# Optimization experiments

Measured on AMD Instinct MI355X. Metric: run time of the kernel, lower is better.

Reference implementation:

```python
import jax, jax.numpy as jnp
import numpy as np

B, S, N, D = 4, 4, 2048, 2048  # batch, residual streams, seq len, model dim


def rmsnorm(x, gamma, eps=1e-12):
    # F.normalize(x, dim=-1) * sqrt(d) * (gamma + 1)
    n = jnp.sqrt(jnp.sum(x * x, axis=-1, keepdims=True))
    return x / jnp.maximum(n, eps) * (x.shape[-1] ** 0.5) * (gamma + 1.0)


def setup_inputs() -> dict:
    key = jax.random.key(0)
    k0, k1, k2, k3 = jax.random.split(key, 4)
    residuals = jax.random.normal(k0, (B * S, N, D), dtype=jnp.float32)
    gamma = (jax.random.normal(k1, (D,), dtype=jnp.float32) * 0.02)
    # ProjActScale weights are zero-init in the module; use small random values
    # so the dynamic paths are numerically exercised.
    w_alpha = jax.random.normal(k2, (S + 1, D), dtype=jnp.float32) * 0.02
    w_beta = jax.random.normal(k3, (1, D), dtype=jnp.float32) * 0.02
    scale_alpha = jnp.asarray(0.01, dtype=jnp.float32)
    scale_beta = jnp.asarray(0.01, dtype=jnp.float32)
    # static_alpha = cat([init_alpha0, eye(S)], dim=1), layer_index=0 -> one-hot row 0
    init_alpha0 = np.zeros((S, 1), dtype=np.float32)
    init_alpha0[0, 0] = 1.0
    static_alpha = jnp.asarray(np.concatenate([init_alpha0, np.eye(S, dtype=np.float32)], axis=1))
    static_beta = jnp.ones((S,), dtype=jnp.float32)
    return dict(residuals=residuals, gamma=gamma, w_alpha=w_alpha, scale_alpha=scale_alpha,
                static_alpha=static_alpha, w_beta=w_beta, scale_beta=scale_beta,
                static_beta=static_beta)


def reference(residuals, gamma, w_alpha, scale_alpha, static_alpha, w_beta, scale_beta, static_beta):
    bs, n, d = residuals.shape
    s = static_beta.shape[0]
    b = bs // s
    # '(b s) n d -> b n s d'
    x = residuals.reshape(b, s, n, d).transpose(0, 2, 1, 3)
    normed = rmsnorm(x, gamma)
    # dynamic alpha / beta: zero-bias linear -> tanh -> scale
    dyn_alpha = jnp.tanh(jnp.einsum('bnsd,td->bnst', normed, w_alpha)) * scale_alpha
    alpha = dyn_alpha + static_alpha                      # (b, n, s, s+1)
    dyn_beta = jnp.tanh(jnp.einsum('bnsd,od->bnso', normed, w_beta))[..., 0] * scale_beta
    beta = dyn_beta + static_beta                         # (b, n, s)
    # width connection: mix residual streams
    mix = jnp.einsum('bnst,bnsd->bntd', alpha, x)         # (b, n, s+1, d)
    branch_input = mix[:, :, 0, :]                        # (b, n, d)
    res = mix[:, :, 1:, :]                                # (b, n, s, d)
    # identity branch (module has branch=None; the add_residual closure applies this)
    branch_out = branch_input
    # depth connection: outer product with beta, add residuals
    res = branch_out[:, :, None, :] * beta[..., None] + res
    # 'b n s d -> (b s) n d'
    out = res.transpose(0, 2, 1, 3).reshape(bs, n, d)
    return out
```

## Files before the change

### kernel.cpp

```cpp
#include <hip/hip_runtime.h>
#include <math.h>

#define NB 4
#define NS 4
#define NN 2048
#define ND 2048
#define NTHREADS 256
#define SQRT_D 45.254833995939045f

typedef float f32x4 __attribute__((ext_vector_type(4)));

#if __has_builtin(__builtin_amdgcn_global_load_lds)
#define HAVE_DMA 1
typedef __attribute__((address_space(3))) void lds_void_t;
typedef const __attribute__((address_space(1))) void glb_void_t;
#define ASYNC_COPY16(g, l) \
    __builtin_amdgcn_global_load_lds((glb_void_t*)(g), (lds_void_t*)(l), 16, 0, 0)
#else
#define HAVE_DMA 0
#endif

#define SHIP(I, H, M_) {                                      \
    const float keep_ = hi_ ? v[(I)+(H)] : v[(I)];            \
    const float give_ = hi_ ? v[(I)] : v[(I)+(H)];            \
    v[(I)] = keep_ + __shfl_xor(give_, (M_)); }

__global__ __launch_bounds__(NTHREADS, 4)
void hyperconn_kernel(const float* __restrict__ residuals,
                      const float* __restrict__ gamma,
                      const float* __restrict__ w_alpha,
                      const float* __restrict__ scale_alpha,
                      const float* __restrict__ static_alpha,
                      const float* __restrict__ w_beta,
                      const float* __restrict__ scale_beta,
                      const float* __restrict__ static_beta,
                      float* __restrict__ out)
{
    __shared__ float lds_x[NS * ND];
    __shared__ float red[4][32];
    __shared__ float asb[NS][6];

    const int tid  = threadIdx.x;
    const int bn   = blockIdx.x;
    const int b    = bn >> 11;
    const int n    = bn & (NN - 1);
    const int wave = tid >> 6;
    const int lane = tid & 63;
    const int d0   = tid << 2;
    const int d1   = d0 + (ND >> 1);

    const size_t row_stride = (size_t)NN * ND;
    const float* xrow = residuals + (size_t)(b * NS + wave) * row_stride + (size_t)n * ND;

#if HAVE_DMA
#pragma unroll
    for (int i = 0; i < 8; ++i) {
        ASYNC_COPY16(xrow + i * 256 + lane * 4, &lds_x[wave * ND + i * 256]);
    }
#else
    {
        f32x4 t[8];
#pragma unroll
        for (int i = 0; i < 8; ++i)
            t[i] = *(const f32x4*)(xrow + i * 256 + lane * 4);
#pragma unroll
        for (int i = 0; i < 8; ++i)
            *(f32x4*)&lds_x[wave * ND + i * 256 + lane * 4] = t[i];
    }
#endif
    __syncthreads();

    float v[32];
#pragma unroll
    for (int k = 0; k < 32; ++k) v[k] = 0.f;

#pragma unroll
    for (int c = 0; c < 2; ++c) {
        const int d = (c == 0) ? d0 : d1;
        f32x4 g4 = *(const f32x4*)(gamma + d);
        f32x4 wg[6];
#pragma unroll
        for (int j = 0; j < 6; ++j) {
            const float* wsrc = (j < 5) ? (w_alpha + (size_t)j * ND + d) : (w_beta + d);
            f32x4 w4 = *(const f32x4*)wsrc;
            wg[j] = w4 + w4 * g4;
        }
#pragma unroll
        for (int s = 0; s < NS; ++s) {
            f32x4 xs = *(const f32x4*)&lds_x[s * ND + d];
#pragma unroll
            for (int e = 0; e < 4; ++e) {
                v[s * 7 + 0] = __builtin_fmaf(xs[e], xs[e], v[s * 7 + 0]);
#pragma unroll
                for (int j = 0; j < 6; ++j)
                    v[s * 7 + 1 + j] = __builtin_fmaf(xs[e], wg[j][e], v[s * 7 + 1 + j]);
            }
        }
    }

    { const bool hi_ = (lane & 1) != 0;
      SHIP(0,16,1)  SHIP(1,16,1)  SHIP(2,16,1)  SHIP(3,16,1)
      SHIP(4,16,1)  SHIP(5,16,1)  SHIP(6,16,1)  SHIP(7,16,1)
      SHIP(8,16,1)  SHIP(9,16,1)  SHIP(10,16,1) SHIP(11,16,1)
      SHIP(12,16,1) SHIP(13,16,1) SHIP(14,16,1) SHIP(15,16,1) }
    { const bool hi_ = (lane & 2) != 0;
      SHIP(0,8,2) SHIP(1,8,2) SHIP(2,8,2) SHIP(3,8,2)
      SHIP(4,8,2) SHIP(5,8,2) SHIP(6,8,2) SHIP(7,8,2) }
    { const bool hi_ = (lane & 4) != 0;
      SHIP(0,4,4) SHIP(1,4,4) SHIP(2,4,4) SHIP(3,4,4) }
    { const bool hi_ = (lane & 8) != 0;
      SHIP(0,2,8) SHIP(1,2,8) }
    { const bool hi_ = (lane & 16) != 0;
      SHIP(0,1,16) }
    const float tot = v[0] + __shfl_xor(v[0], 32);
    const int idx = ((lane & 1) << 4) | ((lane & 2) << 2) | (lane & 4)
                  | ((lane & 8) >> 2) | ((lane & 16) >> 4);
    if (lane < 32) red[wave][idx] = tot;
    __syncthreads();

    if (tid < 24) {
        const int s = tid / 6;
        const int j = tid % 6;
        const float ssq = red[0][s * 7] + red[1][s * 7] + red[2][s * 7] + red[3][s * 7];
        const float dot = red[0][s * 7 + 1 + j] + red[1][s * 7 + 1 + j]
                        + red[2][s * 7 + 1 + j] + red[3][s * 7 + 1 + j];
        const float rs  = SQRT_D / fmaxf(sqrtf(ssq), 1e-12f);
        const float th  = tanhf(dot * rs);
        asb[s][j] = (j < 5) ? (th * scale_alpha[0] + static_alpha[s * 5 + j])
                            : (th * scale_beta[0]  + static_beta[s]);
    }
    __syncthreads();

    float M[NS][NS];
#pragma unroll
    for (int so = 0; so < NS; ++so)
#pragma unroll
        for (int si = 0; si < NS; ++si)
            M[so][si] = asb[so][5] * asb[si][0] + asb[si][so + 1];

    float* obase = out + (size_t)(b * NS) * row_stride + (size_t)n * ND;
#pragma unroll
    for (int c = 0; c < 2; ++c) {
        const int d = (c == 0) ? d0 : d1;
        f32x4 xs0 = *(const f32x4*)&lds_x[0 * ND + d];
        f32x4 xs1 = *(const f32x4*)&lds_x[1 * ND + d];
        f32x4 xs2 = *(const f32x4*)&lds_x[2 * ND + d];
        f32x4 xs3 = *(const f32x4*)&lds_x[3 * ND + d];
#pragma unroll
        for (int so = 0; so < NS; ++so) {
            f32x4 o;
#pragma unroll
            for (int e = 0; e < 4; ++e)
                o[e] = M[so][0] * xs0[e] + M[so][1] * xs1[e]
                     + M[so][2] * xs2[e] + M[so][3] * xs3[e];
            __builtin_nontemporal_store(o, (f32x4*)(obase + (size_t)so * row_stride + d));
        }
    }
}

extern "C" void kernel_launch(void* const* d_in, const int* in_sizes, int n_in,
                              void* d_out, int out_size, void* d_ws, size_t ws_size,
                              hipStream_t stream) {
    const float* residuals    = (const float*)d_in[0];
    const float* gamma        = (const float*)d_in[1];
    const float* w_alpha      = (const float*)d_in[2];
    const float* scale_alpha  = (const float*)d_in[3];
    const float* static_alpha = (const float*)d_in[4];
    const float* w_beta       = (const float*)d_in[5];
    const float* scale_beta   = (const float*)d_in[6];
    const float* static_beta  = (const float*)d_in[7];
    float* out = (float*)d_out;

    const int grid = NB * NN;
    hyperconn_kernel<<<grid, NTHREADS, 0, stream>>>(
        residuals, gamma, w_alpha, scale_alpha, static_alpha,
        w_beta, scale_beta, static_beta, out);
}
```

Measured before the change: 87.80 us.

## Give each wave private LDS columns and compute mixing coefficients redundantly per wave

The load is remapped so each wave copies and later reads only its own column range of all four streams. This lets the block-wide barrier after the async copy become a per-wave vmcnt wait. The final coefficient step no longer has thread 0..23 write to shared memory behind a second barrier. Every wave now computes the 24 coefficients itself and broadcasts them with shuffles, trading a little redundant tanh and shuffle work for one fewer block-wide sync.

```diff
diff --git a/kernel.cpp b/kernel.cpp
--- a/kernel.cpp
+++ b/kernel.cpp
@@ -38,7 +38,6 @@
 {
     __shared__ float lds_x[NS * ND];
     __shared__ float red[4][32];
-    __shared__ float asb[NS][6];
 
     const int tid  = threadIdx.x;
     const int bn   = blockIdx.x;
@@ -46,29 +45,41 @@
     const int n    = bn & (NN - 1);
     const int wave = tid >> 6;
     const int lane = tid & 63;
-    const int d0   = tid << 2;
-    const int d1   = d0 + (ND >> 1);
+    const int d0   = (wave << 9) + (lane << 2);
+    const int d1   = d0 + 256;
 
     const size_t row_stride = (size_t)NN * ND;
-    const float* xrow = residuals + (size_t)(b * NS + wave) * row_stride + (size_t)n * ND;
+    const float* xbase = residuals + (size_t)(b * NS) * row_stride + (size_t)n * ND;
+
+    const int l24 = (lane < 24) ? lane : 0;
+    const int es = l24 / 6, ej = l24 % 6;
+    const float sa = scale_alpha[0], sb = scale_beta[0];
+    const float stat = (ej < 5) ? static_alpha[es * 5 + ej] : static_beta[es];
 
 #if HAVE_DMA
 #pragma unroll
-    for (int i = 0; i < 8; ++i) {
-        ASYNC_COPY16(xrow + i * 256 + lane * 4, &lds_x[wave * ND + i * 256]);
+    for (int s = 0; s < NS; ++s) {
+        const float* g = xbase + (size_t)s * row_stride + (wave << 9) + (lane << 2);
+        ASYNC_COPY16(g,       &lds_x[s * ND + (wave << 9)]);
+        ASYNC_COPY16(g + 256, &lds_x[s * ND + (wave << 9) + 256]);
     }
 #else
     {
         f32x4 t[8];
 #pragma unroll
-        for (int i = 0; i < 8; ++i)
-            t[i] = *(const f32x4*)(xrow + i * 256 + lane * 4);
+        for (int s = 0; s < NS; ++s) {
+            const float* g = xbase + (size_t)s * row_stride + (wave << 9) + (lane << 2);
+            t[s * 2 + 0] = *(const f32x4*)(g);
+            t[s * 2 + 1] = *(const f32x4*)(g + 256);
+        }
 #pragma unroll
-        for (int i = 0; i < 8; ++i)
-            *(f32x4*)&lds_x[wave * ND + i * 256 + lane * 4] = t[i];
+        for (int s = 0; s < NS; ++s) {
+            *(f32x4*)&lds_x[s * ND + d0] = t[s * 2 + 0];
+            *(f32x4*)&lds_x[s * ND + d1] = t[s * 2 + 1];
+        }
     }
 #endif
-    __syncthreads();
+    asm volatile("s_waitcnt vmcnt(0)" ::: "memory");
 
     float v[32];
 #pragma unroll
@@ -118,25 +129,23 @@
     if (lane < 32) red[wave][idx] = tot;
     __syncthreads();
 
-    if (tid < 24) {
-        const int s = tid / 6;
-        const int j = tid % 6;
-        const float ssq = red[0][s * 7] + red[1][s * 7] + red[2][s * 7] + red[3][s * 7];
-        const float dot = red[0][s * 7 + 1 + j] + red[1][s * 7 + 1 + j]
-                        + red[2][s * 7 + 1 + j] + red[3][s * 7 + 1 + j];
-        const float rs  = SQRT_D / fmaxf(sqrtf(ssq), 1e-12f);
-        const float th  = tanhf(dot * rs);
-        asb[s][j] = (j < 5) ? (th * scale_alpha[0] + static_alpha[s * 5 + j])
-                            : (th * scale_beta[0]  + static_beta[s]);
+    const float ssq = red[0][es * 7] + red[1][es * 7] + red[2][es * 7] + red[3][es * 7];
+    const int  di  = es * 7 + 1 + ej;
+    const float dt  = red[0][di] + red[1][di] + red[2][di] + red[3][di];
+    const float rs  = SQRT_D / fmaxf(sqrtf(ssq), 1e-12f);
+    const float aval = __builtin_fmaf(tanhf(dt * rs), (ej < 5) ? sa : sb, stat);
+
+    float a0[4];
+#pragma unroll
+    for (int si = 0; si < 4; ++si) a0[si] = __shfl(aval, si * 6);
+    float M[4][4];
+#pragma unroll
+    for (int so = 0; so < 4; ++so) {
+        const float bso = __shfl(aval, so * 6 + 5);
+#pragma unroll
+        for (int si = 0; si < 4; ++si)
+            M[so][si] = __builtin_fmaf(bso, a0[si], __shfl(aval, si * 6 + so + 1));
     }
-    __syncthreads();
-
-    float M[NS][NS];
-#pragma unroll
-    for (int so = 0; so < NS; ++so)
-#pragma unroll
-        for (int si = 0; si < NS; ++si)
-            M[so][si] = asb[so][5] * asb[si][0] + asb[si][so + 1];
 
     float* obase = out + (size_t)(b * NS) * row_stride + (size_t)n * ND;
 #pragma unroll
@@ -147,7 +156,7 @@
         f32x4 xs2 = *(const f32x4*)&lds_x[2 * ND + d];
         f32x4 xs3 = *(const f32x4*)&lds_x[3 * ND + d];
 #pragma unroll
-        for (int so = 0; so < NS; ++so) {
+        for (int so = 0; so < 4; ++so) {
             f32x4 o;
 #pragma unroll
             for (int e = 0; e < 4; ++e)
```

Result: slower. 94.56 us (+7.7%).

## Load residuals directly to registers and stage them in LDS as bf16

Applied to the files above, without the earlier changes.

Removes the async global-to-LDS DMA and the barrier before compute. Each thread now loads its own four-stream slice straight into registers and accumulates the norms and projections from there. It also writes a bf16-packed copy to LDS for the final mixing pass, halving LDS use from 32KB to 16KB per block so more blocks can fit per CU. The cost is that the output mix is computed from bf16-rounded residuals, which loses precision relative to the fp32 reference.

```diff
diff --git a/kernel.cpp b/kernel.cpp
--- a/kernel.cpp
+++ b/kernel.cpp
@@ -10,20 +10,60 @@
 
 typedef float f32x4 __attribute__((ext_vector_type(4)));
 
-#if __has_builtin(__builtin_amdgcn_global_load_lds)
-#define HAVE_DMA 1
-typedef __attribute__((address_space(3))) void lds_void_t;
-typedef const __attribute__((address_space(1))) void glb_void_t;
-#define ASYNC_COPY16(g, l) \
-    __builtin_amdgcn_global_load_lds((glb_void_t*)(g), (lds_void_t*)(l), 16, 0, 0)
-#else
-#define HAVE_DMA 0
-#endif
+#define CVTPK(dst, a, b) \
+    asm("v_cvt_pk_bf16_f32 %0, %1, %2" : "=v"(dst) : "v"(a), "v"(b))
+
+static __device__ __forceinline__ float bflo(unsigned int u) {
+    unsigned int t = u << 16; float f; __builtin_memcpy(&f, &t, 4); return f;
+}
+static __device__ __forceinline__ float bfhi(unsigned int u) {
+    unsigned int t = u & 0xFFFF0000u; float f; __builtin_memcpy(&f, &t, 4); return f;
+}
 
 #define SHIP(I, H, M_) {                                      \
     const float keep_ = hi_ ? v[(I)+(H)] : v[(I)];            \
     const float give_ = hi_ ? v[(I)] : v[(I)+(H)];            \
     v[(I)] = keep_ + __shfl_xor(give_, (M_)); }
+
+#define CHUNK(DARG)                                                          \
+  {                                                                          \
+    const int d_ = (DARG);                                                   \
+    const float* xp_ = xbase + d_;                                           \
+    f32x4 x0 = *(const f32x4*)(xp_);                                         \
+    f32x4 x1 = *(const f32x4*)(xp_ + row_stride);                            \
+    f32x4 x2 = *(const f32x4*)(xp_ + 2 * row_stride);                        \
+    f32x4 x3 = *(const f32x4*)(xp_ + 3 * row_stride);                        \
+    f32x4 g4 = *(const f32x4*)(gamma + d_);                                  \
+    _Pragma("unroll") for (int e = 0; e < 4; ++e) {                          \
+        v[0]  = __builtin_fmaf(x0[e], x0[e], v[0]);                          \
+        v[7]  = __builtin_fmaf(x1[e], x1[e], v[7]);                          \
+        v[14] = __builtin_fmaf(x2[e], x2[e], v[14]);                         \
+        v[21] = __builtin_fmaf(x3[e], x3[e], v[21]);                         \
+    }                                                                        \
+    {                                                                        \
+        unsigned int pa, pb;                                                 \
+        CVTPK(pa, x0[0], x0[1]); CVTPK(pb, x0[2], x0[3]);                    \
+        *(uint2*)&lds_h[0 * ND + d_] = make_uint2(pa, pb);                   \
+        CVTPK(pa, x1[0], x1[1]); CVTPK(pb, x1[2], x1[3]);                    \
+        *(uint2*)&lds_h[1 * ND + d_] = make_uint2(pa, pb);                   \
+        CVTPK(pa, x2[0], x2[1]); CVTPK(pb, x2[2], x2[3]);                    \
+        *(uint2*)&lds_h[2 * ND + d_] = make_uint2(pa, pb);                   \
+        CVTPK(pa, x3[0], x3[1]); CVTPK(pb, x3[2], x3[3]);                    \
+        *(uint2*)&lds_h[3 * ND + d_] = make_uint2(pa, pb);                   \
+    }                                                                        \
+    _Pragma("unroll") for (int j = 0; j < 6; ++j) {                          \
+        const float* wsrc = (j < 5) ? (w_alpha + (size_t)j * ND + d_)        \
+                                    : (w_beta + d_);                         \
+        f32x4 w4 = *(const f32x4*)wsrc;                                      \
+        f32x4 wg = w4 + w4 * g4;                        \
+        _Pragma("unroll") for (int e = 0; e < 4; ++e) {                      \
+            v[1 + j]  = __builtin_fmaf(x0[e], wg[e], v[1 + j]);              \
+            v[8 + j]  = __builtin_fmaf(x1[e], wg[e], v[8 + j]);              \
+            v[15 + j] = __builtin_fmaf(x2[e], wg[e], v[15 + j]);             \
+            v[22 + j] = __builtin_fmaf(x3[e], wg[e], v[22 + j]);             \
+        }                                                                    \
+    }                                                                        \
+  }
 
 __global__ __launch_bounds__(NTHREADS, 4)
 void hyperconn_kernel(const float* __restrict__ residuals,
@@ -36,7 +76,7 @@
                       const float* __restrict__ static_beta,
                       float* __restrict__ out)
 {
-    __shared__ float lds_x[NS * ND];
+    __shared__ unsigned short lds_h[NS * ND];
     __shared__ float red[4][32];
     __shared__ float asb[NS][6];
 
@@ -50,53 +90,14 @@
     const int d1   = d0 + (ND >> 1);
 
     const size_t row_stride = (size_t)NN * ND;
-    const float* xrow = residuals + (size_t)(b * NS + wave) * row_stride + (size_t)n * ND;
-
-#if HAVE_DMA
-#pragma unroll
-    for (int i = 0; i < 8; ++i) {
-        ASYNC_COPY16(xrow + i * 256 + lane * 4, &lds_x[wave * ND + i * 256]);
-    }
-#else
-    {
-        f32x4 t[8];
-#pragma unroll
-        for (int i = 0; i < 8; ++i)
-            t[i] = *(const f32x4*)(xrow + i * 256 + lane * 4);
-#pragma unroll
-        for (int i = 0; i < 8; ++i)
-            *(f32x4*)&lds_x[wave * ND + i * 256 + lane * 4] = t[i];
-    }
-#endif
-    __syncthreads();
+    const float* xbase = residuals + (size_t)(b * NS) * row_stride + (size_t)n * ND;
 
     float v[32];
 #pragma unroll
     for (int k = 0; k < 32; ++k) v[k] = 0.f;
 
-#pragma unroll
-    for (int c = 0; c < 2; ++c) {
-        const int d = (c == 0) ? d0 : d1;
-        f32x4 g4 = *(const f32x4*)(gamma + d);
-        f32x4 wg[6];
-#pragma unroll
-        for (int j = 0; j < 6; ++j) {
-            const float* wsrc = (j < 5) ? (w_alpha + (size_t)j * ND + d) : (w_beta + d);
-            f32x4 w4 = *(const f32x4*)wsrc;
-            wg[j] = w4 + w4 * g4;
-        }
-#pragma unroll
-        for (int s = 0; s < NS; ++s) {
-            f32x4 xs = *(const f32x4*)&lds_x[s * ND + d];
-#pragma unroll
-            for (int e = 0; e < 4; ++e) {
-                v[s * 7 + 0] = __builtin_fmaf(xs[e], xs[e], v[s * 7 + 0]);
-#pragma unroll
-                for (int j = 0; j < 6; ++j)
-                    v[s * 7 + 1 + j] = __builtin_fmaf(xs[e], wg[j][e], v[s * 7 + 1 + j]);
-            }
-        }
-    }
+    CHUNK(d0)
+    CHUNK(d1)
 
     { const bool hi_ = (lane & 1) != 0;
       SHIP(0,16,1)  SHIP(1,16,1)  SHIP(2,16,1)  SHIP(3,16,1)
@@ -142,10 +143,14 @@
 #pragma unroll
     for (int c = 0; c < 2; ++c) {
         const int d = (c == 0) ? d0 : d1;
-        f32x4 xs0 = *(const f32x4*)&lds_x[0 * ND + d];
-        f32x4 xs1 = *(const f32x4*)&lds_x[1 * ND + d];
-        f32x4 xs2 = *(const f32x4*)&lds_x[2 * ND + d];
-        f32x4 xs3 = *(const f32x4*)&lds_x[3 * ND + d];
+        uint2 q0 = *(uint2*)&lds_h[0 * ND + d];
+        uint2 q1 = *(uint2*)&lds_h[1 * ND + d];
+        uint2 q2 = *(uint2*)&lds_h[2 * ND + d];
+        uint2 q3 = *(uint2*)&lds_h[3 * ND + d];
+        f32x4 xs0 = {bflo(q0.x), bfhi(q0.x), bflo(q0.y), bfhi(q0.y)};
+        f32x4 xs1 = {bflo(q1.x), bfhi(q1.x), bflo(q1.y), bfhi(q1.y)};
+        f32x4 xs2 = {bflo(q2.x), bfhi(q2.x), bflo(q2.y), bfhi(q2.y)};
+        f32x4 xs3 = {bflo(q3.x), bfhi(q3.x), bflo(q3.y), bfhi(q3.y)};
 #pragma unroll
         for (int so = 0; so < NS; ++so) {
             f32x4 o;
```

Result: faster. 84.60 us (-3.7%).

## Drop LDS staging, use 512 threads and reload residuals from global for output

Applied to the files above, without the earlier changes.

Removes the LDS buffer and async global-to-LDS copies. Each of 512 threads now loads one float4 per stream straight into registers for the reductions, then reloads the same values from global (expected to hit L2/MALL) after the reduction barriers to compute the mixed outputs. This frees LDS and raises threads per block and the occupancy hint, but reads the input twice from the memory hierarchy and gives up the software-managed staging.

```diff
diff --git a/kernel.cpp b/kernel.cpp
--- a/kernel.cpp
+++ b/kernel.cpp
@@ -5,27 +5,17 @@
 #define NS 4
 #define NN 2048
 #define ND 2048
-#define NTHREADS 256
+#define NTHREADS 512
 #define SQRT_D 45.254833995939045f
 
 typedef float f32x4 __attribute__((ext_vector_type(4)));
-
-#if __has_builtin(__builtin_amdgcn_global_load_lds)
-#define HAVE_DMA 1
-typedef __attribute__((address_space(3))) void lds_void_t;
-typedef const __attribute__((address_space(1))) void glb_void_t;
-#define ASYNC_COPY16(g, l) \
-    __builtin_amdgcn_global_load_lds((glb_void_t*)(g), (lds_void_t*)(l), 16, 0, 0)
-#else
-#define HAVE_DMA 0
-#endif
 
 #define SHIP(I, H, M_) {                                      \
     const float keep_ = hi_ ? v[(I)+(H)] : v[(I)];            \
     const float give_ = hi_ ? v[(I)] : v[(I)+(H)];            \
     v[(I)] = keep_ + __shfl_xor(give_, (M_)); }
 
-__global__ __launch_bounds__(NTHREADS, 4)
+__global__ __launch_bounds__(NTHREADS, 8)
 void hyperconn_kernel(const float* __restrict__ residuals,
                       const float* __restrict__ gamma,
                       const float* __restrict__ w_alpha,
@@ -36,8 +26,7 @@
                       const float* __restrict__ static_beta,
                       float* __restrict__ out)
 {
-    __shared__ float lds_x[NS * ND];
-    __shared__ float red[4][32];
+    __shared__ float red[8][32];
     __shared__ float asb[NS][6];
 
     const int tid  = threadIdx.x;
@@ -46,54 +35,41 @@
     const int n    = bn & (NN - 1);
     const int wave = tid >> 6;
     const int lane = tid & 63;
-    const int d0   = tid << 2;
-    const int d1   = d0 + (ND >> 1);
+    const int d    = tid << 2;
 
     const size_t row_stride = (size_t)NN * ND;
-    const float* xrow = residuals + (size_t)(b * NS + wave) * row_stride + (size_t)n * ND;
-
-#if HAVE_DMA
-#pragma unroll
-    for (int i = 0; i < 8; ++i) {
-        ASYNC_COPY16(xrow + i * 256 + lane * 4, &lds_x[wave * ND + i * 256]);
-    }
-#else
-    {
-        f32x4 t[8];
-#pragma unroll
-        for (int i = 0; i < 8; ++i)
-            t[i] = *(const f32x4*)(xrow + i * 256 + lane * 4);
-#pragma unroll
-        for (int i = 0; i < 8; ++i)
-            *(f32x4*)&lds_x[wave * ND + i * 256 + lane * 4] = t[i];
-    }
-#endif
-    __syncthreads();
+    const float* xp = residuals + (size_t)(b * NS) * row_stride + (size_t)n * ND + d;
+    float*       op = out       + (size_t)(b * NS) * row_stride + (size_t)n * ND + d;
 
     float v[32];
 #pragma unroll
     for (int k = 0; k < 32; ++k) v[k] = 0.f;
 
+    {
+        f32x4 x0 = *(const f32x4*)(xp);
+        f32x4 x1 = *(const f32x4*)(xp + row_stride);
+        f32x4 x2 = *(const f32x4*)(xp + 2 * row_stride);
+        f32x4 x3 = *(const f32x4*)(xp + 3 * row_stride);
+        f32x4 g4 = *(const f32x4*)(gamma + d);
 #pragma unroll
-    for (int c = 0; c < 2; ++c) {
-        const int d = (c == 0) ? d0 : d1;
-        f32x4 g4 = *(const f32x4*)(gamma + d);
-        f32x4 wg[6];
+        for (int e = 0; e < 4; ++e) {
+            v[0]  = __builtin_fmaf(x0[e], x0[e], v[0]);
+            v[7]  = __builtin_fmaf(x1[e], x1[e], v[7]);
+            v[14] = __builtin_fmaf(x2[e], x2[e], v[14]);
+            v[21] = __builtin_fmaf(x3[e], x3[e], v[21]);
+        }
 #pragma unroll
         for (int j = 0; j < 6; ++j) {
-            const float* wsrc = (j < 5) ? (w_alpha + (size_t)j * ND + d) : (w_beta + d);
+            const float* wsrc = (j < 5) ? (w_alpha + (size_t)j * ND + d)
+                                        : (w_beta + d);
             f32x4 w4 = *(const f32x4*)wsrc;
-            wg[j] = w4 + w4 * g4;
-        }
-#pragma unroll
-        for (int s = 0; s < NS; ++s) {
-            f32x4 xs = *(const f32x4*)&lds_x[s * ND + d];
+            f32x4 wg = w4 + w4 * g4;
 #pragma unroll
             for (int e = 0; e < 4; ++e) {
-                v[s * 7 + 0] = __builtin_fmaf(xs[e], xs[e], v[s * 7 + 0]);
-#pragma unroll
-                for (int j = 0; j < 6; ++j)
-                    v[s * 7 + 1 + j] = __builtin_fmaf(xs[e], wg[j][e], v[s * 7 + 1 + j]);
+                v[1 + j]  = __builtin_fmaf(x0[e], wg[e], v[1 + j]);
+                v[8 + j]  = __builtin_fmaf(x1[e], wg[e], v[8 + j]);
+                v[15 + j] = __builtin_fmaf(x2[e], wg[e], v[15 + j]);
+                v[22 + j] = __builtin_fmaf(x3[e], wg[e], v[22 + j]);
             }
         }
     }
@@ -121,40 +97,39 @@
     if (tid < 24) {
         const int s = tid / 6;
         const int j = tid % 6;
-        const float ssq = red[0][s * 7] + red[1][s * 7] + red[2][s * 7] + red[3][s * 7];
-        const float dot = red[0][s * 7 + 1 + j] + red[1][s * 7 + 1 + j]
-                        + red[2][s * 7 + 1 + j] + red[3][s * 7 + 1 + j];
-        const float rs  = SQRT_D / fmaxf(sqrtf(ssq), 1e-12f);
-        const float th  = tanhf(dot * rs);
+        float ssq = 0.f, dot = 0.f;
+#pragma unroll
+        for (int w = 0; w < 8; ++w) {
+            ssq += red[w][s * 7];
+            dot += red[w][s * 7 + 1 + j];
+        }
+        const float rs = SQRT_D / fmaxf(sqrtf(ssq), 1e-12f);
+        const float th = tanhf(dot * rs);
         asb[s][j] = (j < 5) ? (th * scale_alpha[0] + static_alpha[s * 5 + j])
                             : (th * scale_beta[0]  + static_beta[s]);
     }
     __syncthreads();
+
+    f32x4 y0 = *(const f32x4*)(xp);
+    f32x4 y1 = *(const f32x4*)(xp + row_stride);
+    f32x4 y2 = *(const f32x4*)(xp + 2 * row_stride);
+    f32x4 y3 = *(const f32x4*)(xp + 3 * row_stride);
 
     float M[NS][NS];
 #pragma unroll
     for (int so = 0; so < NS; ++so)
 #pragma unroll
         for (int si = 0; si < NS; ++si)
-            M[so][si] = asb[so][5] * asb[si][0] + asb[si][so + 1];
+            M[so][si] = __builtin_fmaf(asb[so][5], asb[si][0], asb[si][so + 1]);
 
-    float* obase = out + (size_t)(b * NS) * row_stride + (size_t)n * ND;
 #pragma unroll
-    for (int c = 0; c < 2; ++c) {
-        const int d = (c == 0) ? d0 : d1;
-        f32x4 xs0 = *(const f32x4*)&lds_x[0 * ND + d];
-        f32x4 xs1 = *(const f32x4*)&lds_x[1 * ND + d];
-        f32x4 xs2 = *(const f32x4*)&lds_x[2 * ND + d];
-        f32x4 xs3 = *(const f32x4*)&lds_x[3 * ND + d];
+    for (int so = 0; so < NS; ++so) {
+        f32x4 o;
 #pragma unroll
-        for (int so = 0; so < NS; ++so) {
-            f32x4 o;
-#pragma unroll
-            for (int e = 0; e < 4; ++e)
-                o[e] = M[so][0] * xs0[e] + M[so][1] * xs1[e]
-                     + M[so][2] * xs2[e] + M[so][3] * xs3[e];
-            __builtin_nontemporal_store(o, (f32x4*)(obase + (size_t)so * row_stride + d));
-        }
+        for (int e = 0; e < 4; ++e)
+            o[e] = M[so][0] * y0[e] + M[so][1] * y1[e]
+                 + M[so][2] * y2[e] + M[so][3] * y3[e];
+        __builtin_nontemporal_store(o, (f32x4*)(op + (size_t)so * row_stride));
     }
 }
 
```

Measured after the change: 108.0 us. +23.0%, slower.
